# Optimization experiments

Hardware: AMD Instinct MI355X
Metric: run time of the kernel (lower is better)

The kernel has to match this reference:

```python
import jax, jax.numpy as jnp
import numpy as np

# Config (matches init_kwargs)
B, S = 2, 2048            # 2 packed sequences of 2048 tokens (prefill)
HQ, HK, D = 32, 8, 128    # GQA: 32 query heads, 8 kv heads
G = HQ // HK              # group size 4
WINDOW = 1024             # sliding window
THETA = 10000.0


def setup_inputs() -> dict:
    key = jax.random.key(0)
    kq, kk, kv = jax.random.split(key, 3)
    n_tokens = B * S
    query = jax.random.normal(kq, (n_tokens, HQ * D), dtype=jnp.float32)
    key_t = jax.random.normal(kk, (n_tokens, HK * D), dtype=jnp.float32)
    value = jax.random.normal(kv, (n_tokens, HK * D), dtype=jnp.float32)
    # per-sequence positions restart at 0 for each packed sequence
    positions = jnp.tile(jnp.arange(S, dtype=jnp.int32), B)
    return {"query": query, "key": key_t, "value": value, "positions": positions}


def _rope(x, positions):
    # x: [B, S, H, D]; rotate-half (NeoX) RoPE
    half = D // 2
    inv_freq = 1.0 / (THETA ** (jnp.arange(0, half, dtype=jnp.float32) / half))
    ang = positions.astype(jnp.float32)[:, None] * inv_freq[None, :]   # [B*S, D/2]
    cos = jnp.cos(ang).reshape(B, S, 1, half)
    sin = jnp.sin(ang).reshape(B, S, 1, half)
    x1, x2 = x[..., :half], x[..., half:]
    return jnp.concatenate([x1 * cos - x2 * sin, x2 * cos + x1 * sin], axis=-1)


def reference(query, key, value, positions):
    q = query.reshape(B, S, HQ, D)
    k = key.reshape(B, S, HK, D)
    v = value.reshape(B, S, HK, D)
    q = _rope(q, positions)
    k = _rope(k, positions)
    # GQA: split q heads into [HK, G]
    qg = q.reshape(B, S, HK, G, D)
    scale = 1.0 / jnp.sqrt(jnp.float32(D))
    # scores: [B, HK, G, Sq, Skv]
    scores = jnp.einsum('bqhgd,bshd->bhgqs', qg, k) * scale
    i = jnp.arange(S)[:, None]
    j = jnp.arange(S)[None, :]
    # causal + sliding window: j <= i and i - j < WINDOW
    mask = (j <= i) & ((i - j) < WINDOW)
    scores = jnp.where(mask[None, None, None], scores, jnp.float32(-1e30))
    attn = jax.nn.softmax(scores, axis=-1)
    out = jnp.einsum('bhgqs,bshd->bqhgd', attn, v)   # [B, Sq, HK, G, D]
    return out.reshape(B * S, HQ * D)
```

## Files before the change

kernel.cpp:

```cpp
#include <hip/hip_runtime.h>
#include <stdint.h>

#define NB 2
#define NS 2048
#define NHK 8
#define ND 128
#define NWIN 1024

using bf16x8 = __bf16 __attribute__((ext_vector_type(8)));
using f32x4  = float  __attribute__((ext_vector_type(4)));
using f32x2  = float  __attribute__((ext_vector_type(2)));
using f32x8  = float  __attribute__((ext_vector_type(8)));
using u16x8  = unsigned short __attribute__((ext_vector_type(8)));
using u32x4  = unsigned int   __attribute__((ext_vector_type(4)));

#define L2_10K (13.287712379549449f / 64.0f)
#define MASKV (-3.0e38f)

static __device__ __forceinline__ float ex2(float x) {
  return __builtin_amdgcn_exp2f(x);
}

static __device__ __forceinline__ unsigned short f2bf(float x) {
  unsigned int u = __builtin_bit_cast(unsigned int, x);
  u += 0x7FFFu + ((u >> 16) & 1u);
  return (unsigned short)(u >> 16);
}

static __device__ __forceinline__ unsigned int cvtpk(float lo, float hi) {
  unsigned int r;
  asm("v_cvt_pk_bf16_f32 %0, %1, %2" : "=v"(r) : "v"(lo), "v"(hi));
  return r;
}

static __device__ __forceinline__ void gll16(const void* g, void* l) {
  __builtin_amdgcn_global_load_lds(
      (const __attribute__((address_space(1))) void*)g,
      (__attribute__((address_space(3))) void*)l, 16, 0, 0);
}

#define MFMA16(a, b, c) __builtin_amdgcn_mfma_f32_16x16x32_bf16((a), (b), (c), 0, 0, 0)

__global__ __launch_bounds__(64) void build_tab(float* __restrict__ tab) {
  const int p = blockIdx.x, f = threadIdx.x;
  float s, c;
  __sincosf((float)p * ex2(-(float)f * L2_10K), &s, &c);
  tab[(size_t)p * 128 + f] = c;
  tab[(size_t)p * 128 + 64 + f] = s;
}

__global__ __launch_bounds__(256) void prepass(
    const float* __restrict__ kin, const float* __restrict__ vin,
    const int* __restrict__ pos, const float* __restrict__ tab,
    unsigned short* __restrict__ kimg, unsigned short* __restrict__ vimg) {
  const int bid = blockIdx.x;
  const int ti = bid & 63, gidx = bid >> 6;
  const int hk = gidx & 7, b = gidx >> 3;
  const int t = threadIdx.x;

  unsigned short* kout = kimg + (size_t)bid * 4096;
#pragma unroll
  for (int uu = 0; uu < 2; ++uu) {
    const int u = t * 2 + uu;
    const int j = u >> 4;
    const int d0 = ((u & 15) << 3) ^ ((j & 7) << 3);
    const int tok = (b << 11) + (ti << 5) + j;
    const float* kp = kin + (size_t)tok * (NHK * ND) + hk * ND;
    f32x8 a = *(const f32x8*)(kp + d0);
    f32x8 p = *(const f32x8*)(kp + (d0 ^ 64));
    const float* tr = tab + (size_t)(pos[tok] & 2047) * 128 + (d0 & 63);
    f32x8 c8 = *(const f32x8*)tr;
    f32x8 s8 = *(const f32x8*)(tr + 64);
    u16x8 o;
#pragma unroll
    for (int i = 0; i < 8; ++i) {
      float val = (d0 < 64) ? (a[i] * c8[i] - p[i] * s8[i])
                            : (a[i] * c8[i] + p[i] * s8[i]);
      o[i] = f2bf(val);
    }
    *(u16x8*)(kout + (size_t)u * 8) = o;
  }

  unsigned short* vout = vimg + (size_t)bid * 4096;
  {
    const int d0 = (t >> 2) << 1;
    const int kp4 = t & 3;
    const int tok0 = (b << 11) + (ti << 5) + (kp4 << 3);
    const float* vp = vin + (size_t)tok0 * (NHK * ND) + hk * ND + d0;
    u16x8 lo, hi;
#pragma unroll
    for (int i = 0; i < 8; ++i) {
      f32x2 r = *(const f32x2*)(vp + (size_t)i * (NHK * ND));
      lo[i] = f2bf(r[0]);
      hi[i] = f2bf(r[1]);
    }
    const int sub = kp4 ^ ((d0 >> 1) & 3);
    *(u16x8*)(vout + d0 * 32 + sub * 8) = lo;
    *(u16x8*)(vout + (d0 + 1) * 32 + sub * 8) = hi;
  }
}

template <bool PRE>
__global__ __launch_bounds__(256, 3) void attn_fwd(
    const float* __restrict__ qin, const float* __restrict__ kin,
    const float* __restrict__ vin, const int* __restrict__ pos,
    const char* __restrict__ kimg, const char* __restrict__ vimg,
    const float* __restrict__ tab, float* __restrict__ out) {
  __shared__ __align__(16) char Kb[2][8192];

  const int B = blockIdx.x;
  const int group = (B & 7) + ((B >> 9) << 3);
  const int qt = 63 - ((B >> 3) & 63);
  const int hk = group & 7, b = group >> 3;

  const int tid = threadIdx.x;
  const int w = tid >> 6, lane = tid & 63, h = lane >> 4, ln = lane & 15;
  const int g = w;
  const int q0b = qt << 5;
  int lo = q0b - (NWIN - 1);
  if (lo < 0) lo = 0;
  lo &= ~31;
  const int ti0 = lo >> 5;
  const int nt = (q0b >> 5) - ti0 + 1;

  const size_t gbase = (size_t)group * 64 * 8192;
  const char* kg = PRE ? kimg + gbase + (size_t)(w * 128 + lane) * 16 : nullptr;
  const char* vgb = PRE ? vimg + gbase : nullptr;

  auto stage = [&](int sl, int ti) {
    if constexpr (PRE) {
      const char* ksrc = kg + (size_t)ti * 8192;
      char* kd = &Kb[sl][w * 2048];
      gll16(ksrc, kd);
      gll16(ksrc + 1024, kd + 1024);
    } else {
      const int j = tid >> 3;
      const int du = (tid & 7) << 4;
      const int tok = (b << 11) + (ti << 5) + j;
      const float* kp = kin + (size_t)tok * (NHK * ND) + hk * ND;
      const float pj = (float)pos[tok];
#pragma unroll
      for (int gq = 0; gq < 2; ++gq) {
        const int dd = du + gq * 8;
        f32x8 a = *(const f32x8*)(kp + dd);
        f32x8 p = *(const f32x8*)(kp + (dd ^ 64));
        u16x8 o;
#pragma unroll
        for (int i = 0; i < 8; ++i) {
          float s, c;
          __sincosf(pj * ex2(-(float)((dd & 63) + i) * L2_10K), &s, &c);
          float val = (dd < 64) ? (a[i] * c - p[i] * s) : (a[i] * c + p[i] * s);
          o[i] = f2bf(val);
        }
        *(u16x8*)(&Kb[sl][((j << 8) + (dd << 1)) ^ ((j & 7) << 4)]) = o;
      }
    }
  };

  stage(0, ti0);

  const float QSC = 0.08838834764831845f * 1.4426950408889634f;
  bf16x8 qfr[2][4];
#pragma unroll
  for (int hf = 0; hf < 2; ++hf) {
    const int qrow = q0b + hf * 16 + ln;
    const size_t tokq = (size_t)(b << 11) + qrow;
    const float* qp = qin + tokq * 4096 + (hk * 4 + g) * 128;
    const int posq = pos[tokq] & 2047;
#pragma unroll
    for (int pp = 0; pp < 2; ++pp) {
      const int rr = (pp << 5) + (h << 3);
      f32x8 lo8 = *(const f32x8*)(qp + rr);
      f32x8 hi8 = *(const f32x8*)(qp + rr + 64);
      f32x8 cc, ss;
      if constexpr (PRE) {
        const float* tp = tab + (size_t)posq * 128 + rr;
        cc = *(const f32x8*)tp;
        ss = *(const f32x8*)(tp + 64);
      } else {
        const float pf = (float)posq;
#pragma unroll
        for (int i = 0; i < 8; ++i) {
          float s, c;
          __sincosf(pf * ex2(-(float)(rr + i) * L2_10K), &s, &c);
          cc[i] = c;
          ss[i] = s;
        }
      }
      u16x8 ulo, uhi;
#pragma unroll
      for (int i = 0; i < 8; ++i) {
        ulo[i] = f2bf((lo8[i] * cc[i] - hi8[i] * ss[i]) * QSC);
        uhi[i] = f2bf((hi8[i] * cc[i] + lo8[i] * ss[i]) * QSC);
      }
      qfr[hf][pp] = __builtin_bit_cast(bf16x8, ulo);
      qfr[hf][2 + pp] = __builtin_bit_cast(bf16x8, uhi);
    }
  }

  f32x4 Oc[2][8] = {};
  float msh[2] = {-1e30f, -1e30f};
  float lsum[2] = {};
  const int sw = (ln & 7) << 4;
  const int voff = (ln << 6) + ((h ^ ((ln >> 1) & 3)) << 4);

  for (int t = 0; t < nt; ++t) {
    asm volatile("s_waitcnt vmcnt(0)" ::: "memory");
    __syncthreads();
    if (t + 1 < nt) stage((t + 1) & 1, ti0 + t + 1);

    const int j0 = (ti0 + t) << 5;
    const char* KB = Kb[t & 1];
    const char* vt = PRE ? vgb + (size_t)(ti0 + t) * 8192 : nullptr;

    bf16x8 vf[8];
    if constexpr (PRE) {
#pragma unroll
      for (int db = 0; db < 4; ++db)
        vf[db] = *(const bf16x8*)(vt + (db << 10) + voff);
    } else {
#pragma unroll
      for (int db = 0; db < 4; ++db) {
        u16x8 o;
#pragma unroll
        for (int i = 0; i < 8; ++i)
          o[i] = f2bf(vin[(size_t)((b << 11) + j0 + (h << 3) + i) * (NHK * ND) +
                          hk * ND + (db << 4) + ln]);
        vf[db] = __builtin_bit_cast(bf16x8, o);
      }
    }

    f32x4 sT[2][2] = {};
    __builtin_amdgcn_s_setprio(1);
#pragma unroll
    for (int c = 0; c < 4; ++c) {
      const bf16x8 k0 = *(const bf16x8*)(
          KB + (((ln << 8) + (c << 6) + (h << 4)) ^ sw));
      const bf16x8 k1 = *(const bf16x8*)(
          KB + ((((16 + ln) << 8) + (c << 6) + (h << 4)) ^ sw));
      sT[0][0] = MFMA16(k0, qfr[0][c], sT[0][0]);
      sT[0][1] = MFMA16(k1, qfr[0][c], sT[0][1]);
      sT[1][0] = MFMA16(k0, qfr[1][c], sT[1][0]);
      sT[1][1] = MFMA16(k1, qfr[1][c], sT[1][1]);
    }
    __builtin_amdgcn_s_setprio(0);

    if ((j0 >= q0b) || (j0 < q0b - 992)) {
#pragma unroll
      for (int qh = 0; qh < 2; ++qh) {
        const int irow = q0b + qh * 16 + ln;
#pragma unroll
        for (int ki = 0; ki < 2; ++ki)
#pragma unroll
          for (int r = 0; r < 4; ++r) {
            const int j = j0 + ki * 16 + (h << 2) + r;
            if (!(j <= irow && irow - j < NWIN)) sT[qh][ki][r] = MASKV;
          }
      }
    }

    float pm[2];
#pragma unroll
    for (int qh = 0; qh < 2; ++qh) {
      const f32x4 a0 = sT[qh][0], a1 = sT[qh][1];
      pm[qh] = fmaxf(fmaxf(fmaxf(a0[0], a0[1]), fmaxf(a0[2], a0[3])),
                     fmaxf(fmaxf(a1[0], a1[1]), fmaxf(a1[2], a1[3])));
    }
    const float ov = fmaxf(pm[0] - msh[0], pm[1] - msh[1]);
    if (__any(ov > 8.0f)) {
#pragma unroll
      for (int qh = 0; qh < 2; ++qh) {
        float M = pm[qh];
        M = fmaxf(M, __shfl_xor(M, 16));
        M = fmaxf(M, __shfl_xor(M, 32));
        const float mn = fmaxf(msh[qh], M);
        const float co = ex2(msh[qh] - mn);
        msh[qh] = mn;
        lsum[qh] *= co;
        float coO[4];
#pragma unroll
        for (int r = 0; r < 4; ++r) coO[r] = __shfl(co, (h << 2) + r);
#pragma unroll
        for (int db = 0; db < 8; ++db)
#pragma unroll
          for (int r = 0; r < 4; ++r) Oc[qh][db][r] *= coO[r];
      }
    }

    bf16x8 pa[2];
#pragma unroll
    for (int qh = 0; qh < 2; ++qh) {
#pragma unroll
      for (int ki = 0; ki < 2; ++ki)
#pragma unroll
        for (int r = 0; r < 4; ++r)
          sT[qh][ki][r] = ex2(sT[qh][ki][r] - msh[qh]);
      lsum[qh] += ((sT[qh][0][0] + sT[qh][0][1]) + (sT[qh][0][2] + sT[qh][0][3])) +
                  ((sT[qh][1][0] + sT[qh][1][1]) + (sT[qh][1][2] + sT[qh][1][3]));
      unsigned int A = cvtpk(sT[qh][0][0], sT[qh][0][1]);
      unsigned int Bk = cvtpk(sT[qh][0][2], sT[qh][0][3]);
      unsigned int C = cvtpk(sT[qh][1][0], sT[qh][1][1]);
      unsigned int D = cvtpk(sT[qh][1][2], sT[qh][1][3]);
      asm volatile("v_permlane32_swap_b32 %0, %1" : "+v"(A), "+v"(C));
      asm volatile("v_permlane16_swap_b32 %0, %1" : "+v"(A), "+v"(C));
      asm volatile("v_permlane32_swap_b32 %0, %1" : "+v"(Bk), "+v"(D));
      asm volatile("v_permlane16_swap_b32 %0, %1" : "+v"(Bk), "+v"(D));
      u32x4 pk4 = {A, Bk, C, D};
      pa[qh] = __builtin_bit_cast(bf16x8, pk4);
    }

    if constexpr (PRE) {
#pragma unroll
      for (int db = 4; db < 8; ++db)
        vf[db] = *(const bf16x8*)(vt + (db << 10) + voff);
    } else {
#pragma unroll
      for (int db = 4; db < 8; ++db) {
        u16x8 o;
#pragma unroll
        for (int i = 0; i < 8; ++i)
          o[i] = f2bf(vin[(size_t)((b << 11) + j0 + (h << 3) + i) * (NHK * ND) +
                          hk * ND + (db << 4) + ln]);
        vf[db] = __builtin_bit_cast(bf16x8, o);
      }
    }

    __builtin_amdgcn_s_setprio(1);
#pragma unroll
    for (int db = 0; db < 8; ++db) {
      Oc[0][db] = MFMA16(pa[0], vf[db], Oc[0][db]);
      Oc[1][db] = MFMA16(pa[1], vf[db], Oc[1][db]);
    }
    __builtin_amdgcn_s_setprio(0);
  }

#pragma unroll
  for (int qh = 0; qh < 2; ++qh) {
    float ls = lsum[qh];
    ls += __shfl_xor(ls, 16);
    ls += __shfl_xor(ls, 32);
#pragma unroll
    for (int r = 0; r < 4; ++r) {
      const float rl = 1.0f / __shfl(ls, (h << 2) + r);
      const int irow = q0b + qh * 16 + (h << 2) + r;
      float* op = out + ((size_t)(b << 11) + irow) * 4096 + (hk * 4 + g) * 128 + ln;
#pragma unroll
      for (int db = 0; db < 8; ++db) op[db * 16] = Oc[qh][db][r] * rl;
    }
  }
}

extern "C" void kernel_launch(void* const* d_in, const int* in_sizes, int n_in,
                              void* d_out, int out_size, void* d_ws, size_t ws_size,
                              hipStream_t stream) {
  const float* q = (const float*)d_in[0];
  const float* k = (const float*)d_in[1];
  const float* v = (const float*)d_in[2];
  const int* pos = (const int*)d_in[3];
  float* out = (float*)d_out;

  const size_t TAB = (size_t)2048 * 128 * 4;
  const size_t KIMG = (size_t)16 * 64 * 8192;
  const size_t need = TAB + 2 * KIMG;

  if (ws_size >= need) {
    float* tab = (float*)d_ws;
    char* kimg = (char*)d_ws + TAB;
    char* vimg = kimg + KIMG;
    build_tab<<<2048, 64, 0, stream>>>(tab);
    prepass<<<1024, 256, 0, stream>>>(k, v, pos, tab,
                                      (unsigned short*)kimg, (unsigned short*)vimg);
    attn_fwd<true><<<1024, 256, 0, stream>>>(q, k, v, pos, kimg, vimg, tab, out);
  } else {
    attn_fwd<false><<<1024, 256, 0, stream>>>(q, k, v, pos, nullptr, nullptr, nullptr, out);
  }
}
```

Before: 103.3 us.

## Double KV tile to 64 keys and stage V through LDS alongside K

Raises the key tile from 32 to 64 tokens per iteration, halving the number of loop iterations and barriers, and stages V into double-buffered shared memory with async global-to-LDS loads instead of reading V fragments directly from global memory inside the loop. The aim is to cut per-iteration sync and softmax bookkeeping overhead and to hide V load latency behind the pipeline. In exchange, shared memory use grows to 64 KB per block and the launch bound drops from 3 to 2 blocks per CU, reducing occupancy. More masked work is also done at the window edges because of coarser tile alignment.

```diff
diff --git a/kernel.cpp b/kernel.cpp
--- a/kernel.cpp
+++ b/kernel.cpp
@@ -101,12 +101,13 @@
 }
 
 template <bool PRE>
-__global__ __launch_bounds__(256, 3) void attn_fwd(
+__global__ __launch_bounds__(256, 2) void attn_fwd(
     const float* __restrict__ qin, const float* __restrict__ kin,
     const float* __restrict__ vin, const int* __restrict__ pos,
     const char* __restrict__ kimg, const char* __restrict__ vimg,
     const float* __restrict__ tab, float* __restrict__ out) {
-  __shared__ __align__(16) char Kb[2][8192];
+  __shared__ __align__(16) char Kb[2][16384];
+  __shared__ __align__(16) char Vb[2][16384];
 
   const int B = blockIdx.x;
   const int group = (B & 7) + ((B >> 9) << 3);
@@ -119,40 +120,56 @@
   const int q0b = qt << 5;
   int lo = q0b - (NWIN - 1);
   if (lo < 0) lo = 0;
-  lo &= ~31;
-  const int ti0 = lo >> 5;
-  const int nt = (q0b >> 5) - ti0 + 1;
+  lo &= ~63;
+  const int ti0 = lo >> 6;
+  const int nt = (q0b >> 6) - ti0 + 1;
 
   const size_t gbase = (size_t)group * 64 * 8192;
-  const char* kg = PRE ? kimg + gbase + (size_t)(w * 128 + lane) * 16 : nullptr;
-  const char* vgb = PRE ? vimg + gbase : nullptr;
-
-  auto stage = [&](int sl, int ti) {
+  const char* kg = PRE ? kimg + gbase + (size_t)tid * 16 : nullptr;
+  const char* vg = PRE ? vimg + gbase + (size_t)tid * 16 : nullptr;
+
+  auto stage = [&](int sl, int T) {
     if constexpr (PRE) {
-      const char* ksrc = kg + (size_t)ti * 8192;
-      char* kd = &Kb[sl][w * 2048];
-      gll16(ksrc, kd);
-      gll16(ksrc + 1024, kd + 1024);
+      const char* ks = kg + (size_t)T * 16384;
+      const char* vs = vg + (size_t)T * 16384;
+#pragma unroll
+      for (int i = 0; i < 4; ++i) {
+        gll16(ks + i * 4096, &Kb[sl][i * 4096 + (w << 10)]);
+        gll16(vs + i * 4096, &Vb[sl][i * 4096 + (w << 10)]);
+      }
     } else {
-      const int j = tid >> 3;
-      const int du = (tid & 7) << 4;
-      const int tok = (b << 11) + (ti << 5) + j;
+      const int j = tid >> 2;
+      const int tok = (b << 11) + (T << 6) + j;
       const float* kp = kin + (size_t)tok * (NHK * ND) + hk * ND;
       const float pj = (float)pos[tok];
 #pragma unroll
-      for (int gq = 0; gq < 2; ++gq) {
-        const int dd = du + gq * 8;
+      for (int dch = 0; dch < 4; ++dch) {
+        const int dd = ((tid & 3) << 5) + (dch << 3);
+        const int f = dd & 63;
         f32x8 a = *(const f32x8*)(kp + dd);
         f32x8 p = *(const f32x8*)(kp + (dd ^ 64));
         u16x8 o;
 #pragma unroll
         for (int i = 0; i < 8; ++i) {
           float s, c;
-          __sincosf(pj * ex2(-(float)((dd & 63) + i) * L2_10K), &s, &c);
+          __sincosf(pj * ex2(-(float)(f + i) * L2_10K), &s, &c);
           float val = (dd < 64) ? (a[i] * c - p[i] * s) : (a[i] * c + p[i] * s);
           o[i] = f2bf(val);
         }
         *(u16x8*)(&Kb[sl][((j << 8) + (dd << 1)) ^ ((j & 7) << 4)]) = o;
+      }
+      const int d = tid >> 1;
+      const int half = tid & 1;
+      unsigned short* vb16 = (unsigned short*)(Vb[sl] + half * 8192);
+#pragma unroll
+      for (int kp4 = 0; kp4 < 4; ++kp4) {
+        const int tok0 = (b << 11) + (T << 6) + (half << 5) + (kp4 << 3);
+        const float* vp = vin + (size_t)tok0 * (NHK * ND) + hk * ND + d;
+        u16x8 ov;
+#pragma unroll
+        for (int i = 0; i < 8; ++i) ov[i] = f2bf(vp[(size_t)i * (NHK * ND)]);
+        const int sub = kp4 ^ ((d >> 1) & 3);
+        *(u16x8*)(vb16 + d * 32 + sub * 8) = ov;
       }
     }
   };
@@ -202,55 +219,39 @@
   float msh[2] = {-1e30f, -1e30f};
   float lsum[2] = {};
   const int sw = (ln & 7) << 4;
-  const int voff = (ln << 6) + ((h ^ ((ln >> 1) & 3)) << 4);
+  const int vsub = (h ^ ((ln >> 1) & 3)) << 4;
 
   for (int t = 0; t < nt; ++t) {
     asm volatile("s_waitcnt vmcnt(0)" ::: "memory");
     __syncthreads();
     if (t + 1 < nt) stage((t + 1) & 1, ti0 + t + 1);
 
-    const int j0 = (ti0 + t) << 5;
+    const int j0 = (ti0 + t) << 6;
     const char* KB = Kb[t & 1];
-    const char* vt = PRE ? vgb + (size_t)(ti0 + t) * 8192 : nullptr;
-
-    bf16x8 vf[8];
-    if constexpr (PRE) {
-#pragma unroll
-      for (int db = 0; db < 4; ++db)
-        vf[db] = *(const bf16x8*)(vt + (db << 10) + voff);
-    } else {
-#pragma unroll
-      for (int db = 0; db < 4; ++db) {
-        u16x8 o;
-#pragma unroll
-        for (int i = 0; i < 8; ++i)
-          o[i] = f2bf(vin[(size_t)((b << 11) + j0 + (h << 3) + i) * (NHK * ND) +
-                          hk * ND + (db << 4) + ln]);
-        vf[db] = __builtin_bit_cast(bf16x8, o);
-      }
-    }
-
-    f32x4 sT[2][2] = {};
+
+    f32x4 sT[2][4] = {};
     __builtin_amdgcn_s_setprio(1);
 #pragma unroll
     for (int c = 0; c < 4; ++c) {
-      const bf16x8 k0 = *(const bf16x8*)(
-          KB + (((ln << 8) + (c << 6) + (h << 4)) ^ sw));
-      const bf16x8 k1 = *(const bf16x8*)(
-          KB + ((((16 + ln) << 8) + (c << 6) + (h << 4)) ^ sw));
-      sT[0][0] = MFMA16(k0, qfr[0][c], sT[0][0]);
-      sT[0][1] = MFMA16(k1, qfr[0][c], sT[0][1]);
-      sT[1][0] = MFMA16(k0, qfr[1][c], sT[1][0]);
-      sT[1][1] = MFMA16(k1, qfr[1][c], sT[1][1]);
+      bf16x8 kf[4];
+#pragma unroll
+      for (int ki = 0; ki < 4; ++ki)
+        kf[ki] = *(const bf16x8*)(
+            KB + ((((ki * 16 + ln) << 8) + (c << 6) + (h << 4)) ^ sw));
+#pragma unroll
+      for (int ki = 0; ki < 4; ++ki) {
+        sT[0][ki] = MFMA16(kf[ki], qfr[0][c], sT[0][ki]);
+        sT[1][ki] = MFMA16(kf[ki], qfr[1][c], sT[1][ki]);
+      }
     }
     __builtin_amdgcn_s_setprio(0);
 
-    if ((j0 >= q0b) || (j0 < q0b - 992)) {
+    if ((j0 + 63 >= q0b) || (j0 < q0b - 992)) {
 #pragma unroll
       for (int qh = 0; qh < 2; ++qh) {
         const int irow = q0b + qh * 16 + ln;
 #pragma unroll
-        for (int ki = 0; ki < 2; ++ki)
+        for (int ki = 0; ki < 4; ++ki)
 #pragma unroll
           for (int r = 0; r < 4; ++r) {
             const int j = j0 + ki * 16 + (h << 2) + r;
@@ -262,9 +263,15 @@
     float pm[2];
 #pragma unroll
     for (int qh = 0; qh < 2; ++qh) {
-      const f32x4 a0 = sT[qh][0], a1 = sT[qh][1];
-      pm[qh] = fmaxf(fmaxf(fmaxf(a0[0], a0[1]), fmaxf(a0[2], a0[3])),
-                     fmaxf(fmaxf(a1[0], a1[1]), fmaxf(a1[2], a1[3])));
+      float m0 = fmaxf(fmaxf(sT[qh][0][0], sT[qh][0][1]),
+                       fmaxf(sT[qh][0][2], sT[qh][0][3]));
+      float m1 = fmaxf(fmaxf(sT[qh][1][0], sT[qh][1][1]),
+                       fmaxf(sT[qh][1][2], sT[qh][1][3]));
+      float m2 = fmaxf(fmaxf(sT[qh][2][0], sT[qh][2][1]),
+                       fmaxf(sT[qh][2][2], sT[qh][2][3]));
+      float m3 = fmaxf(fmaxf(sT[qh][3][0], sT[qh][3][1]),
+                       fmaxf(sT[qh][3][2], sT[qh][3][3]));
+      pm[qh] = fmaxf(fmaxf(m0, m1), fmaxf(m2, m3));
     }
     const float ov = fmaxf(pm[0] - msh[0], pm[1] - msh[1]);
     if (__any(ov > 8.0f)) {
@@ -287,49 +294,43 @@
       }
     }
 
-    bf16x8 pa[2];
 #pragma unroll
     for (int qh = 0; qh < 2; ++qh) {
 #pragma unroll
-      for (int ki = 0; ki < 2; ++ki)
+      for (int ki = 0; ki < 4; ++ki)
 #pragma unroll
         for (int r = 0; r < 4; ++r)
           sT[qh][ki][r] = ex2(sT[qh][ki][r] - msh[qh]);
-      lsum[qh] += ((sT[qh][0][0] + sT[qh][0][1]) + (sT[qh][0][2] + sT[qh][0][3])) +
-                  ((sT[qh][1][0] + sT[qh][1][1]) + (sT[qh][1][2] + sT[qh][1][3]));
-      unsigned int A = cvtpk(sT[qh][0][0], sT[qh][0][1]);
-      unsigned int Bk = cvtpk(sT[qh][0][2], sT[qh][0][3]);
-      unsigned int C = cvtpk(sT[qh][1][0], sT[qh][1][1]);
-      unsigned int D = cvtpk(sT[qh][1][2], sT[qh][1][3]);
-      asm volatile("v_permlane32_swap_b32 %0, %1" : "+v"(A), "+v"(C));
-      asm volatile("v_permlane16_swap_b32 %0, %1" : "+v"(A), "+v"(C));
-      asm volatile("v_permlane32_swap_b32 %0, %1" : "+v"(Bk), "+v"(D));
-      asm volatile("v_permlane16_swap_b32 %0, %1" : "+v"(Bk), "+v"(D));
-      u32x4 pk4 = {A, Bk, C, D};
-      pa[qh] = __builtin_bit_cast(bf16x8, pk4);
-    }
-
-    if constexpr (PRE) {
-#pragma unroll
-      for (int db = 4; db < 8; ++db)
-        vf[db] = *(const bf16x8*)(vt + (db << 10) + voff);
-    } else {
-#pragma unroll
-      for (int db = 4; db < 8; ++db) {
-        u16x8 o;
-#pragma unroll
-        for (int i = 0; i < 8; ++i)
-          o[i] = f2bf(vin[(size_t)((b << 11) + j0 + (h << 3) + i) * (NHK * ND) +
-                          hk * ND + (db << 4) + ln]);
-        vf[db] = __builtin_bit_cast(bf16x8, o);
-      }
+      lsum[qh] += (((sT[qh][0][0] + sT[qh][0][1]) + (sT[qh][0][2] + sT[qh][0][3])) +
+                   ((sT[qh][1][0] + sT[qh][1][1]) + (sT[qh][1][2] + sT[qh][1][3]))) +
+                  (((sT[qh][2][0] + sT[qh][2][1]) + (sT[qh][2][2] + sT[qh][2][3])) +
+                   ((sT[qh][3][0] + sT[qh][3][1]) + (sT[qh][3][2] + sT[qh][3][3])));
     }
 
     __builtin_amdgcn_s_setprio(1);
 #pragma unroll
-    for (int db = 0; db < 8; ++db) {
-      Oc[0][db] = MFMA16(pa[0], vf[db], Oc[0][db]);
-      Oc[1][db] = MFMA16(pa[1], vf[db], Oc[1][db]);
+    for (int kh = 0; kh < 2; ++kh) {
+      bf16x8 pa[2];
+#pragma unroll
+      for (int qh = 0; qh < 2; ++qh) {
+        unsigned int A = cvtpk(sT[qh][2 * kh][0], sT[qh][2 * kh][1]);
+        unsigned int Bk = cvtpk(sT[qh][2 * kh][2], sT[qh][2 * kh][3]);
+        unsigned int C = cvtpk(sT[qh][2 * kh + 1][0], sT[qh][2 * kh + 1][1]);
+        unsigned int D = cvtpk(sT[qh][2 * kh + 1][2], sT[qh][2 * kh + 1][3]);
+        asm volatile("v_permlane32_swap_b32 %0, %1" : "+v"(A), "+v"(C));
+        asm volatile("v_permlane16_swap_b32 %0, %1" : "+v"(A), "+v"(C));
+        asm volatile("v_permlane32_swap_b32 %0, %1" : "+v"(Bk), "+v"(D));
+        asm volatile("v_permlane16_swap_b32 %0, %1" : "+v"(Bk), "+v"(D));
+        u32x4 pk4 = {A, Bk, C, D};
+        pa[qh] = __builtin_bit_cast(bf16x8, pk4);
+      }
+      const char* VB = Vb[t & 1] + kh * 8192;
+#pragma unroll
+      for (int db = 0; db < 8; ++db) {
+        const bf16x8 vv = *(const bf16x8*)(VB + (db << 10) + (ln << 6) + vsub);
+        Oc[0][db] = MFMA16(pa[0], vv, Oc[0][db]);
+        Oc[1][db] = MFMA16(pa[1], vv, Oc[1][db]);
+      }
     }
     __builtin_amdgcn_s_setprio(0);
   }
```

Result: slower. 109.6 us (+6.1%).
